# Performance work log

Hardware: AMD Instinct MI355X
Metric: run time of the kernel (lower is better)

The kernel has to match this reference:

```python
import jax, jax.numpy as jnp
import numpy as np

ALPHA = 0.2
NOISE_STD = 0.05
I, H, O, R, S, G = 3, 2048, 2, 2, 4, 7
B, T = 32, 512


def _proxies(wi, unitwi, m, n, unitm, unitn, wo, h0, unith0, bias, gb, uv, sup):
    # gb: (G,H) gaussian basis, uv: (1,H) unit vector, sup: (S,H) support masks
    def comb(p, up):  # p: (K,S,G), up: (K,S,1) -> (K,H)
        return jnp.sum((jnp.einsum('ksg,gh->ksh', p, gb) + up * uv) * sup, axis=1)

    wi_full = comb(wi, unitwi)                                          # (I,H)
    m_rec = comb(m, unitm).T                                            # (H,R)
    n_rec = comb(n, unitn).T                                            # (H,R)
    wo_full = jnp.sum(jnp.einsum('osg,gh->osh', wo, gb) * sup, axis=1).T  # (H,O)
    h0_full = jnp.sum((h0 @ gb) * sup, axis=0) + jnp.sum((unith0 * uv) * sup, axis=0)  # (H,)
    bias_full = jnp.sum((bias * uv) * sup, axis=0)                      # (H,)
    w_rec = m_rec @ n_rec.T                                             # (H,H)
    return wi_full, wo_full, w_rec, h0_full, bias_full


def setup_inputs() -> dict:
    key = jax.random.key(0)
    ks = jax.random.split(key, 16)
    sc = 1.0 / np.sqrt(G)
    sup = np.zeros((S, H), dtype=np.float32)
    l = H // S
    for i in range(S):
        sup[i, l * i:l * (i + 1)] = 1.0
    return {
        'input': jax.random.normal(ks[0], (B, T, I), jnp.float32),
        'noise': jax.random.normal(ks[1], (B, T, H), jnp.float32),
        'wi': jax.random.normal(ks[2], (I, S, G), jnp.float32) * sc,
        'unitwi': jax.random.normal(ks[3], (I, S, 1), jnp.float32) * sc,
        'm': jax.random.normal(ks[4], (R, S, G), jnp.float32) * sc,
        'n': jax.random.normal(ks[5], (R, S, G), jnp.float32) * sc,
        'unitm': jax.random.normal(ks[6], (R, S, 1), jnp.float32) * sc,
        'unitn': jax.random.normal(ks[7], (R, S, 1), jnp.float32) * sc,
        'wo': jax.random.normal(ks[8], (O, S, G), jnp.float32) * sc,
        'h0': jax.random.normal(ks[9], (S, G), jnp.float32) * sc,
        'unith0': jax.random.normal(ks[10], (S, 1), jnp.float32) * sc,
        'bias': jax.random.normal(ks[11], (S, 1), jnp.float32) * 0.01,
        'gaussian_basis': jax.random.normal(ks[12], (G, H), jnp.float32),
        'unit_vector': jnp.ones((1, H), jnp.float32),
        'supports': jnp.asarray(sup),
    }


def reference(input, noise, wi, unitwi, m, n, unitm, unitn, wo, h0, unith0, bias,
              gaussian_basis, unit_vector, supports):
    wi_full, wo_full, w_rec, h0_full, bias_full = _proxies(
        wi, unitwi, m, n, unitm, unitn, wo, h0, unith0, bias,
        gaussian_basis, unit_vector, supports)
    batch = input.shape[0]
    h0b = jnp.broadcast_to(h0_full, (batch, h0_full.shape[0]))  # (B,H)

    def step(h, xs):
        x_t, z_t = xs                       # (B,I), (B,H)
        r = jnp.tanh(h)
        h = h + bias_full + NOISE_STD * z_t + ALPHA * (-h + r @ w_rec.T + x_t @ wi_full)
        r = jnp.tanh(h)
        return h, (r @ wo_full, h)

    _, (out, traj) = jax.lax.scan(step, h0b,
                                  (jnp.swapaxes(input, 0, 1), jnp.swapaxes(noise, 0, 1)))
    return jnp.swapaxes(out, 0, 1), jnp.swapaxes(traj, 0, 1)  # (B,T,O), (B,T,H)
```

## Files before the change

kernel.cpp:

```cpp
#include <hip/hip_runtime.h>

constexpr int I_N = 3, H_N = 2048, O_N = 2, S_N = 4, G_N = 7;
constexpr int B_N = 32, T_N = 512;
constexpr int TPB = 512;
constexpr int EPT = H_N / TPB;
constexpr int NWAVE = TPB / 64;
constexpr float ALPHA_C = 0.2f;
constexpr float NSTD_C = 0.05f;

__device__ __forceinline__ float fast_tanh(float x) {
  float e = __expf(2.0f * x);
  return fmaf(-2.0f, __builtin_amdgcn_rcpf(e + 1.0f), 1.0f);
}

#define DPP_ADD(x, ctrl, rmask)                                                  \
  x += __int_as_float(__builtin_amdgcn_update_dpp(                               \
      0, __float_as_int(x), (ctrl), (rmask), 0xf, true))

__device__ __forceinline__ float wave_sum63(float x) {
  DPP_ADD(x, 0x111, 0xf);
  DPP_ADD(x, 0x112, 0xf);
  DPP_ADD(x, 0x114, 0xf);
  DPP_ADD(x, 0x118, 0xf);
  DPP_ADD(x, 0x142, 0xa);
  DPP_ADD(x, 0x143, 0xc);
  return x;
}

__device__ __forceinline__ float rdlane(float v, int l) {
  return __int_as_float(__builtin_amdgcn_readlane(__float_as_int(v), l));
}

__global__ __launch_bounds__(TPB) void rnn_fused(
    const float* __restrict__ input,
    const float* __restrict__ noise,
    const float* __restrict__ wi,
    const float* __restrict__ unitwi,
    const float* __restrict__ m_,
    const float* __restrict__ n_,
    const float* __restrict__ unitm,
    const float* __restrict__ unitn,
    const float* __restrict__ wo,
    const float* __restrict__ h0,
    const float* __restrict__ unith0,
    const float* __restrict__ bias,
    const float* __restrict__ gb,
    const float* __restrict__ uv,
    const float* __restrict__ sup,
    float* __restrict__ out,
    float* __restrict__ traj) {
  const int tid = threadIdx.x;
  const int lane = tid & 63;
  const int wave = tid >> 6;
  const int b = blockIdx.x;
  const int hbase = tid * EPT;
  const int s = hbase >> 9;

  __shared__ float partials[2][NWAVE * 4];

  float cn0[EPT], cn1[EPT], cm0[EPT], cm1[EPT];
  float cw0[EPT], cw1[EPT], cw2[EPT];
  float co0[EPT], co1[EPT], cb[EPT], h[EPT], r[EPT];

  for (int e = 0; e < EPT; ++e) {
    const int hh = hbase + e;
    float gbh[G_N];
#pragma unroll
    for (int g = 0; g < G_N; ++g) gbh[g] = gb[g * H_N + hh];
    const float uvh = uv[hh];
    const float sv = sup[s * H_N + hh];

    auto comb = [&](const float* p, const float* up, int k) {
      float acc = up[k * S_N + s] * uvh;
#pragma unroll
      for (int g = 0; g < G_N; ++g)
        acc = fmaf(p[(k * S_N + s) * G_N + g], gbh[g], acc);
      return acc * sv;
    };
    auto combNoU = [&](const float* p, int k) {
      float acc = 0.0f;
#pragma unroll
      for (int g = 0; g < G_N; ++g)
        acc = fmaf(p[(k * S_N + s) * G_N + g], gbh[g], acc);
      return acc * sv;
    };

    cn0[e] = comb(n_, unitn, 0);
    cn1[e] = comb(n_, unitn, 1);
    cm0[e] = ALPHA_C * comb(m_, unitm, 0);
    cm1[e] = ALPHA_C * comb(m_, unitm, 1);
    cw0[e] = ALPHA_C * comb(wi, unitwi, 0);
    cw1[e] = ALPHA_C * comb(wi, unitwi, 1);
    cw2[e] = ALPHA_C * comb(wi, unitwi, 2);
    co0[e] = combNoU(wo, 0);
    co1[e] = combNoU(wo, 1);
    cb[e] = bias[s] * uvh * sv;
    h[e] = comb(h0, unith0, 0);
    r[e] = fast_tanh(h[e]);
  }

  const float* zp = noise + ((size_t)b * T_N) * H_N + hbase;
  const float* xp = input + ((size_t)b * T_N) * I_N;
  float* tp = traj + ((size_t)b * T_N) * H_N + hbase;
  float* op = out + ((size_t)b * T_N) * O_N;

  float4 zc = *(const float4*)zp;
  float x0 = xp[0], x1 = xp[1], x2 = xp[2];

  __builtin_amdgcn_s_waitcnt(0xC07F);
  __builtin_amdgcn_s_barrier();

#pragma unroll 2
  for (int t = 0; t < T_N; ++t) {
    const int tn = (t + 1 < T_N) ? t + 1 : t;
    float4 zn = *(const float4*)(zp + (size_t)tn * H_N);
    const float* xq = xp + tn * I_N;
    float nx0 = xq[0], nx1 = xq[1], nx2 = xq[2];

    float pa0 = 0.f, pa1 = 0.f, po0 = 0.f, po1 = 0.f;
#pragma unroll
    for (int e = 0; e < EPT; ++e) {
      pa0 = fmaf(r[e], cn0[e], pa0);
      pa1 = fmaf(r[e], cn1[e], pa1);
      po0 = fmaf(r[e], co0[e], po0);
      po1 = fmaf(r[e], co1[e], po1);
    }
    pa0 = wave_sum63(pa0);
    pa1 = wave_sum63(pa1);
    po0 = wave_sum63(po0);
    po1 = wave_sum63(po1);
    const int pb = t & 1;
    if (lane == 63) {
      float4 v4 = make_float4(pa0, pa1, po0, po1);
      *(float4*)&partials[pb][wave * 4] = v4;
    }
    __builtin_amdgcn_s_waitcnt(0xC07F);
    __builtin_amdgcn_s_barrier();

    float v = partials[pb][lane & 31];
    DPP_ADD(v, 0x124, 0xf);
    DPP_ADD(v, 0x128, 0xf);
    v += __int_as_float(__builtin_amdgcn_ds_swizzle(__float_as_int(v), 0x401F));
    const float a0 = rdlane(v, 0);
    const float a1 = rdlane(v, 1);
    const float o0 = rdlane(v, 2);
    const float o1 = rdlane(v, 3);

    if (tid == 0 && t > 0) ((float2*)op)[t - 1] = make_float2(o0, o1);

    float ze[EPT] = {zc.x, zc.y, zc.z, zc.w};
#pragma unroll
    for (int e = 0; e < EPT; ++e) {
      float u = fmaf(NSTD_C, ze[e], cb[e]);
      u = fmaf(x0, cw0[e], u);
      u = fmaf(x1, cw1[e], u);
      u = fmaf(x2, cw2[e], u);
      u = fmaf(a0, cm0[e], u);
      u = fmaf(a1, cm1[e], u);
      h[e] = fmaf(1.0f - ALPHA_C, h[e], u);
    }
    *(float4*)(tp + (size_t)t * H_N) = make_float4(h[0], h[1], h[2], h[3]);
#pragma unroll
    for (int e = 0; e < EPT; ++e) r[e] = fast_tanh(h[e]);

    zc = zn; x0 = nx0; x1 = nx1; x2 = nx2;
  }

  {
    float po0 = 0.f, po1 = 0.f;
#pragma unroll
    for (int e = 0; e < EPT; ++e) {
      po0 = fmaf(r[e], co0[e], po0);
      po1 = fmaf(r[e], co1[e], po1);
    }
    po0 = wave_sum63(po0);
    po1 = wave_sum63(po1);
    if (lane == 63) {
      partials[0][wave * 4 + 2] = po0;
      partials[0][wave * 4 + 3] = po1;
    }
    __builtin_amdgcn_s_waitcnt(0xC07F);
    __builtin_amdgcn_s_barrier();
    if (tid == 0) {
      float o0 = 0.f, o1 = 0.f;
#pragma unroll
      for (int w = 0; w < NWAVE; ++w) {
        o0 += partials[0][w * 4 + 2];
        o1 += partials[0][w * 4 + 3];
      }
      ((float2*)op)[T_N - 1] = make_float2(o0, o1);
    }
  }
}

extern "C" void kernel_launch(void* const* d_in, const int* in_sizes, int n_in,
                              void* d_out, int out_size, void* d_ws, size_t ws_size,
                              hipStream_t stream) {
  const float* input  = (const float*)d_in[0];
  const float* noise  = (const float*)d_in[1];
  const float* wi     = (const float*)d_in[2];
  const float* unitwi = (const float*)d_in[3];
  const float* m_     = (const float*)d_in[4];
  const float* n_     = (const float*)d_in[5];
  const float* unitm  = (const float*)d_in[6];
  const float* unitn  = (const float*)d_in[7];
  const float* wo     = (const float*)d_in[8];
  const float* h0     = (const float*)d_in[9];
  const float* unith0 = (const float*)d_in[10];
  const float* bias   = (const float*)d_in[11];
  const float* gb     = (const float*)d_in[12];
  const float* uv     = (const float*)d_in[13];
  const float* sup    = (const float*)d_in[14];

  float* out  = (float*)d_out;
  float* traj = out + (size_t)B_N * T_N * O_N;

  rnn_fused<<<dim3(B_N), dim3(TPB), 0, stream>>>(
      input, noise, wi, unitwi, m_, n_, unitm, unitn, wo, h0, unith0, bias,
      gb, uv, sup, out, traj);
}
```

Baseline: 488.5 us.

## Reduce via LDS atomics with triple-buffered accumulators and packed FMA math

The per-step cross-wave reduction now uses a 16-lane DPP row reduction followed by LDS float atomics into a triple-buffered float4 accumulator. This drops the second post-barrier DPP/swizzle/readlane stage, while a single thread zeros the buffer two steps ahead. The input-projection terms are moved ahead of the barrier and computed with packed v2f FMAs. Inputs x are staged in LDS, noise is prefetched two steps ahead, and tanh uses exp2 directly. The cost is 32 LDS atomic adds per value per step, which may serialize, and float-atomic ordering makes the sums nondeterministic.

```diff
diff --git a/kernel.cpp b/kernel.cpp
--- a/kernel.cpp
+++ b/kernel.cpp
@@ -1,35 +1,23 @@
 #include <hip/hip_runtime.h>
+
+typedef float v2f __attribute__((ext_vector_type(2)));
 
 constexpr int I_N = 3, H_N = 2048, O_N = 2, S_N = 4, G_N = 7;
 constexpr int B_N = 32, T_N = 512;
 constexpr int TPB = 512;
 constexpr int EPT = H_N / TPB;
-constexpr int NWAVE = TPB / 64;
 constexpr float ALPHA_C = 0.2f;
 constexpr float NSTD_C = 0.05f;
+constexpr float TWO_LOG2E = 2.885390081777927f;
 
 __device__ __forceinline__ float fast_tanh(float x) {
-  float e = __expf(2.0f * x);
+  float e = __builtin_amdgcn_exp2f(x * TWO_LOG2E);
   return fmaf(-2.0f, __builtin_amdgcn_rcpf(e + 1.0f), 1.0f);
 }
 
-#define DPP_ADD(x, ctrl, rmask)                                                  \
-  x += __int_as_float(__builtin_amdgcn_update_dpp(                               \
-      0, __float_as_int(x), (ctrl), (rmask), 0xf, true))
-
-__device__ __forceinline__ float wave_sum63(float x) {
-  DPP_ADD(x, 0x111, 0xf);
-  DPP_ADD(x, 0x112, 0xf);
-  DPP_ADD(x, 0x114, 0xf);
-  DPP_ADD(x, 0x118, 0xf);
-  DPP_ADD(x, 0x142, 0xa);
-  DPP_ADD(x, 0x143, 0xc);
-  return x;
-}
-
-__device__ __forceinline__ float rdlane(float v, int l) {
-  return __int_as_float(__builtin_amdgcn_readlane(__float_as_int(v), l));
-}
+#define DPP_ADD(x, ctrl)                                                       \
+  x += __int_as_float(__builtin_amdgcn_update_dpp(                             \
+      0, __float_as_int(x), (ctrl), 0xf, 0xf, true))
 
 __global__ __launch_bounds__(TPB) void rnn_fused(
     const float* __restrict__ input,
@@ -51,16 +39,16 @@
     float* __restrict__ traj) {
   const int tid = threadIdx.x;
   const int lane = tid & 63;
-  const int wave = tid >> 6;
   const int b = blockIdx.x;
   const int hbase = tid * EPT;
   const int s = hbase >> 9;
 
-  __shared__ float partials[2][NWAVE * 4];
+  __shared__ float4 bufs[3];
+  __shared__ float4 xs4[T_N];
 
   float cn0[EPT], cn1[EPT], cm0[EPT], cm1[EPT];
   float cw0[EPT], cw1[EPT], cw2[EPT];
-  float co0[EPT], co1[EPT], cb[EPT], h[EPT], r[EPT];
+  float co0[EPT], co1[EPT], cb[EPT], hh_[EPT], r[EPT];
 
   for (int e = 0; e < EPT; ++e) {
     const int hh = hbase + e;
@@ -95,100 +83,145 @@
     co0[e] = combNoU(wo, 0);
     co1[e] = combNoU(wo, 1);
     cb[e] = bias[s] * uvh * sv;
-    h[e] = comb(h0, unith0, 0);
-    r[e] = fast_tanh(h[e]);
-  }
+    hh_[e] = comb(h0, unith0, 0);
+    r[e] = fast_tanh(hh_[e]);
+  }
+
+  v2f cnp[EPT], cop[EPT];
+  v2f cm0p[2], cm1p[2], cw0p[2], cw1p[2], cw2p[2], cbp[2];
+#pragma unroll
+  for (int e = 0; e < EPT; ++e) {
+    cnp[e] = (v2f){cn0[e], cn1[e]};
+    cop[e] = (v2f){co0[e], co1[e]};
+  }
+#pragma unroll
+  for (int p2 = 0; p2 < 2; ++p2) {
+    cm0p[p2] = (v2f){cm0[2 * p2], cm0[2 * p2 + 1]};
+    cm1p[p2] = (v2f){cm1[2 * p2], cm1[2 * p2 + 1]};
+    cw0p[p2] = (v2f){cw0[2 * p2], cw0[2 * p2 + 1]};
+    cw1p[p2] = (v2f){cw1[2 * p2], cw1[2 * p2 + 1]};
+    cw2p[p2] = (v2f){cw2[2 * p2], cw2[2 * p2 + 1]};
+    cbp[p2] = (v2f){cb[2 * p2], cb[2 * p2 + 1]};
+  }
+  v2f h01 = (v2f){hh_[0], hh_[1]};
+  v2f h23 = (v2f){hh_[2], hh_[3]};
 
   const float* zp = noise + ((size_t)b * T_N) * H_N + hbase;
   const float* xp = input + ((size_t)b * T_N) * I_N;
   float* tp = traj + ((size_t)b * T_N) * H_N + hbase;
   float* op = out + ((size_t)b * T_N) * O_N;
 
-  float4 zc = *(const float4*)zp;
-  float x0 = xp[0], x1 = xp[1], x2 = xp[2];
+  {
+    const float* xq = xp + tid * I_N;
+    xs4[tid] = make_float4(xq[0], xq[1], xq[2], 0.0f);
+  }
+  if (tid == 0) {
+    bufs[0] = make_float4(0.f, 0.f, 0.f, 0.f);
+    bufs[1] = make_float4(0.f, 0.f, 0.f, 0.f);
+  }
+
+  float4 z0 = *(const float4*)zp;
+  float4 z1 = *(const float4*)(zp + H_N);
 
   __builtin_amdgcn_s_waitcnt(0xC07F);
   __builtin_amdgcn_s_barrier();
+  __asm__ volatile("" ::: "memory");
+
+  float4 xv = xs4[0];
+  int pb = 0, pz = 2;
 
 #pragma unroll 2
   for (int t = 0; t < T_N; ++t) {
-    const int tn = (t + 1 < T_N) ? t + 1 : t;
-    float4 zn = *(const float4*)(zp + (size_t)tn * H_N);
-    const float* xq = xp + tn * I_N;
-    float nx0 = xq[0], nx1 = xq[1], nx2 = xq[2];
-
-    float pa0 = 0.f, pa1 = 0.f, po0 = 0.f, po1 = 0.f;
+    const int tz = (t + 2 < T_N) ? t + 2 : T_N - 1;
+    float4 zn = *(const float4*)(zp + (size_t)tz * H_N);
+    const int tx = (t + 1 < T_N) ? t + 1 : T_N - 1;
+    float4 xn = xs4[tx];
+
+    v2f z01 = (v2f){z0.x, z0.y}, z23 = (v2f){z0.z, z0.w};
+    v2f pre01 = cbp[0];
+    pre01 += NSTD_C * z01;
+    pre01 += xv.x * cw0p[0];
+    pre01 += xv.y * cw1p[0];
+    pre01 += xv.z * cw2p[0];
+    v2f pre23 = cbp[1];
+    pre23 += NSTD_C * z23;
+    pre23 += xv.x * cw0p[1];
+    pre23 += xv.y * cw1p[1];
+    pre23 += xv.z * cw2p[1];
+
+    v2f accA = (v2f){0.f, 0.f}, accO = (v2f){0.f, 0.f};
 #pragma unroll
     for (int e = 0; e < EPT; ++e) {
-      pa0 = fmaf(r[e], cn0[e], pa0);
-      pa1 = fmaf(r[e], cn1[e], pa1);
-      po0 = fmaf(r[e], co0[e], po0);
-      po1 = fmaf(r[e], co1[e], po1);
-    }
-    pa0 = wave_sum63(pa0);
-    pa1 = wave_sum63(pa1);
-    po0 = wave_sum63(po0);
-    po1 = wave_sum63(po1);
-    const int pb = t & 1;
-    if (lane == 63) {
-      float4 v4 = make_float4(pa0, pa1, po0, po1);
-      *(float4*)&partials[pb][wave * 4] = v4;
+      v2f rr = (v2f){r[e], r[e]};
+      accA += rr * cnp[e];
+      accO += rr * cop[e];
+    }
+    float pa0 = accA.x, pa1 = accA.y, po0 = accO.x, po1 = accO.y;
+
+    DPP_ADD(pa0, 0x111); DPP_ADD(pa0, 0x112); DPP_ADD(pa0, 0x114); DPP_ADD(pa0, 0x118);
+    DPP_ADD(pa1, 0x111); DPP_ADD(pa1, 0x112); DPP_ADD(pa1, 0x114); DPP_ADD(pa1, 0x118);
+    DPP_ADD(po0, 0x111); DPP_ADD(po0, 0x112); DPP_ADD(po0, 0x114); DPP_ADD(po0, 0x118);
+    DPP_ADD(po1, 0x111); DPP_ADD(po1, 0x112); DPP_ADD(po1, 0x114); DPP_ADD(po1, 0x118);
+
+    float* bp = (float*)&bufs[pb];
+    if ((lane & 15) == 15) {
+      atomicAdd(bp + 0, pa0);
+      atomicAdd(bp + 1, pa1);
+      atomicAdd(bp + 2, po0);
+      atomicAdd(bp + 3, po1);
     }
     __builtin_amdgcn_s_waitcnt(0xC07F);
     __builtin_amdgcn_s_barrier();
-
-    float v = partials[pb][lane & 31];
-    DPP_ADD(v, 0x124, 0xf);
-    DPP_ADD(v, 0x128, 0xf);
-    v += __int_as_float(__builtin_amdgcn_ds_swizzle(__float_as_int(v), 0x401F));
-    const float a0 = rdlane(v, 0);
-    const float a1 = rdlane(v, 1);
-    const float o0 = rdlane(v, 2);
-    const float o1 = rdlane(v, 3);
-
-    if (tid == 0 && t > 0) ((float2*)op)[t - 1] = make_float2(o0, o1);
-
-    float ze[EPT] = {zc.x, zc.y, zc.z, zc.w};
+    __asm__ volatile("" ::: "memory");
+
+    const float4 res = *(const float4*)&bufs[pb];
+    const float a0 = res.x, a1 = res.y;
+
+    if (tid == 0) {
+      if (t > 0) ((float2*)op)[t - 1] = make_float2(res.z, res.w);
+      bufs[pz] = make_float4(0.f, 0.f, 0.f, 0.f);
+    }
+
+    h01 = 0.8f * h01 + pre01;
+    h01 += a0 * cm0p[0];
+    h01 += a1 * cm1p[0];
+    h23 = 0.8f * h23 + pre23;
+    h23 += a0 * cm0p[1];
+    h23 += a1 * cm1p[1];
+
+    *(float4*)(tp + (size_t)t * H_N) = make_float4(h01.x, h01.y, h23.x, h23.y);
+
+    r[0] = fast_tanh(h01.x);
+    r[1] = fast_tanh(h01.y);
+    r[2] = fast_tanh(h23.x);
+    r[3] = fast_tanh(h23.y);
+
+    z0 = z1; z1 = zn; xv = xn;
+    pb = (pb == 2) ? 0 : pb + 1;
+    pz = (pz == 2) ? 0 : pz + 1;
+  }
+
+  {
+    v2f accO = (v2f){0.f, 0.f};
 #pragma unroll
     for (int e = 0; e < EPT; ++e) {
-      float u = fmaf(NSTD_C, ze[e], cb[e]);
-      u = fmaf(x0, cw0[e], u);
-      u = fmaf(x1, cw1[e], u);
-      u = fmaf(x2, cw2[e], u);
-      u = fmaf(a0, cm0[e], u);
-      u = fmaf(a1, cm1[e], u);
-      h[e] = fmaf(1.0f - ALPHA_C, h[e], u);
-    }
-    *(float4*)(tp + (size_t)t * H_N) = make_float4(h[0], h[1], h[2], h[3]);
-#pragma unroll
-    for (int e = 0; e < EPT; ++e) r[e] = fast_tanh(h[e]);
-
-    zc = zn; x0 = nx0; x1 = nx1; x2 = nx2;
-  }
-
-  {
-    float po0 = 0.f, po1 = 0.f;
-#pragma unroll
-    for (int e = 0; e < EPT; ++e) {
-      po0 = fmaf(r[e], co0[e], po0);
-      po1 = fmaf(r[e], co1[e], po1);
-    }
-    po0 = wave_sum63(po0);
-    po1 = wave_sum63(po1);
-    if (lane == 63) {
-      partials[0][wave * 4 + 2] = po0;
-      partials[0][wave * 4 + 3] = po1;
+      v2f rr = (v2f){r[e], r[e]};
+      accO += rr * cop[e];
+    }
+    float po0 = accO.x, po1 = accO.y;
+    DPP_ADD(po0, 0x111); DPP_ADD(po0, 0x112); DPP_ADD(po0, 0x114); DPP_ADD(po0, 0x118);
+    DPP_ADD(po1, 0x111); DPP_ADD(po1, 0x112); DPP_ADD(po1, 0x114); DPP_ADD(po1, 0x118);
+    float* bp = (float*)&bufs[pb];
+    if ((lane & 15) == 15) {
+      atomicAdd(bp + 2, po0);
+      atomicAdd(bp + 3, po1);
     }
     __builtin_amdgcn_s_waitcnt(0xC07F);
     __builtin_amdgcn_s_barrier();
+    __asm__ volatile("" ::: "memory");
     if (tid == 0) {
-      float o0 = 0.f, o1 = 0.f;
-#pragma unroll
-      for (int w = 0; w < NWAVE; ++w) {
-        o0 += partials[0][w * 4 + 2];
-        o1 += partials[0][w * 4 + 3];
-      }
-      ((float2*)op)[T_N - 1] = make_float2(o0, o1);
+      const float4 res = *(const float4*)&bufs[pb];
+      ((float2*)op)[T_N - 1] = make_float2(res.z, res.w);
     }
   }
 }
```

New measurement: 934.0 us. 91.2% more time.
